# Kernel optimization log

Measured on AMD Instinct MI355X. Metric: run time of the kernel, lower is better.

The kernel has to match this reference:

```python
import jax, jax.numpy as jnp
import numpy as np

B, T, N, M = 128, 128, 32, 128  # batch, window(input_len), driving_series, hidden_size


def _lstm_cell(x_t, h, c, Wih, Whh, bih, bhh):
    # PyTorch gate order: i, f, g, o
    g = x_t @ Wih.T + bih + h @ Whh.T + bhh
    i, f, gg, o = jnp.split(g, 4, axis=-1)
    c = jax.nn.sigmoid(f) * c + jax.nn.sigmoid(i) * jnp.tanh(gg)
    h = jax.nn.sigmoid(o) * jnp.tanh(c)
    return h, c


def _lstm_seq(x, Wih, Whh, bih, bhh):
    # x: [B,T,n] -> outputs [B,T,m], zero init state
    Bc = x.shape[0]
    m = Whh.shape[1]
    def step(carry, x_t):
        h, c = carry
        h, c = _lstm_cell(x_t, h, c, Wih, Whh, bih, bhh)
        return (h, c), h
    h0 = jnp.zeros((Bc, m), x.dtype)
    (_, _), ys = jax.lax.scan(step, (h0, h0), jnp.swapaxes(x, 0, 1))
    return jnp.swapaxes(ys, 0, 1)


def _forward(x, Wih0, Whh0, bih0, bhh0, We, Ue, Ve,
             Wg, bg, Wa, ba,
             Wih1, Whh1, bih1, bhh1, Wih2, Whh2, bih2, bhh2):
    Bc, Tc, n = x.shape
    m = Whh0.shape[1]
    ux = jnp.einsum('btn,mn->btm', x, Ue)  # Ue(x), constant across steps

    def step(carry, x_t):
        h, c = carry
        hs = jnp.concatenate([h, c], axis=-1)              # [B,2m]
        e = jnp.tanh(ux + (hs @ We.T)[:, None, :]) @ Ve[0]  # [B,T]
        a = jax.nn.softmax(e, axis=1)
        ia_t = jnp.einsum('bt,btn->bn', a, x)              # attended input at step t
        h, c = _lstm_cell(x_t, h, c, Wih0, Whh0, bih0, bhh0)
        return (h, c), ia_t

    h0 = jnp.zeros((Bc, m), x.dtype)
    (_, _), ia = jax.lax.scan(step, (h0, h0), jnp.swapaxes(x, 0, 1))
    input_attention = jnp.swapaxes(ia, 0, 1)               # [B,T,n]

    # self (spatial) attention, fully vectorized over t
    g = jnp.tanh(jnp.einsum('btn,mn->btm', x, Wg) + bg)
    a = jax.nn.sigmoid(jnp.einsum('btm,nm->btn', g, Wa) + ba)
    self_attention = a * x                                  # [B,T,n]

    out1 = _lstm_seq(input_attention, Wih1, Whh1, bih1, bhh1)
    out2 = _lstm_seq(self_attention, Wih2, Whh2, bih2, bhh2)
    return jnp.concatenate([out1, out2], axis=-1)           # [B,T,2m]


def setup_inputs() -> dict:
    key = jax.random.key(0)
    ks = jax.random.split(key, 20)
    stdv = 1.0 / np.sqrt(M)
    u = lambda k, shp: jax.random.uniform(k, shp, jnp.float32, -stdv, stdv)
    inp = {
        'x': jax.random.normal(ks[0], (B, T, N), jnp.float32),
        'Wih0': u(ks[1], (4 * M, N)), 'Whh0': u(ks[2], (4 * M, M)),
        'bih0': u(ks[3], (4 * M,)), 'bhh0': u(ks[4], (4 * M,)),
        'We': u(ks[5], (M, 2 * M)), 'Ue': u(ks[6], (M, N)), 'Ve': u(ks[7], (1, M)),
        'Wg': u(ks[8], (M, N)), 'bg': u(ks[9], (M,)),
        'Wa': u(ks[10], (N, M)), 'ba': u(ks[11], (N,)),
        'Wih1': u(ks[12], (4 * M, N)), 'Whh1': u(ks[13], (4 * M, M)),
        'bih1': u(ks[14], (4 * M,)), 'bhh1': u(ks[15], (4 * M,)),
        'Wih2': u(ks[16], (4 * M, N)), 'Whh2': u(ks[17], (4 * M, M)),
        'bih2': u(ks[18], (4 * M,)), 'bhh2': u(ks[19], (4 * M,)),
    }
    return inp


def reference(x, Wih0, Whh0, bih0, bhh0, We, Ue, Ve, Wg, bg, Wa, ba,
              Wih1, Whh1, bih1, bhh1, Wih2, Whh2, bih2, bhh2):
    return _forward(x, Wih0, Whh0, bih0, bhh0, We, Ue, Ve, Wg, bg, Wa, ba,
                    Wih1, Whh1, bih1, bhh1, Wih2, Whh2, bih2, bhh2)
```

## Files before the change

kernel.cpp:

```cpp
#include <hip/hip_runtime.h>

#define DI __device__ __forceinline__

typedef _Float16 h2v __attribute__((ext_vector_type(2)));

DI float frcp(float v)  { return __builtin_amdgcn_rcpf(v); }
DI float fexp2(float v) { return __builtin_amdgcn_exp2f(v); }
DI float fsig(float v)  { return frcp(1.0f + __expf(-v)); }
DI float ftanh(float v) { return 1.0f - 2.0f * frcp(__expf(2.0f * v) + 1.0f); }
DI float dot4(float4 a, float4 b) { return a.x*b.x + a.y*b.y + a.z*b.z + a.w*b.w; }

DI h2v u2h(unsigned u) { return __builtin_bit_cast(h2v, u); }
DI unsigned pkrtz(float a, float b) {
    return __builtin_bit_cast(unsigned, __builtin_amdgcn_cvt_pkrtz(a, b));
}

DI float fdot2w(h2v a, h2v b, float c) {
#if __has_builtin(__builtin_amdgcn_fdot2)
    return __builtin_amdgcn_fdot2(a, b, c, false);
#else
    return c + (float)a.x * (float)b.x + (float)a.y * (float)b.y;
#endif
}

#define TWO_LOG2E 2.8853900817779268f

template <int MODE>
DI void lstm_scan4(const float* __restrict__ xin,
                   const float* __restrict__ Wih,
                   const float* __restrict__ Whh,
                   const float* __restrict__ bih,
                   const float* __restrict__ bhh,
                   float* __restrict__ rec,
                   float* __restrict__ outp,
                   float* lds)
{
    const int tid = threadIdx.x;
    const int r0 = tid & 127;
    const int kq = tid >> 7;
    unsigned* xp = (unsigned*)lds;
    unsigned* hp = (unsigned*)lds + 2048;
    float* pl = lds + 2112;

    for (int i = tid; i < 2048; i += 512) {
        const float2 v = *(const float2*)(xin + 2 * i);
        xp[i] = pkrtz(v.x, v.y);
    }
    if (tid < 64) hp[tid] = 0u;

    unsigned wpu[4][20];
    #pragma unroll
    for (int g = 0; g < 4; ++g) {
        const int r = g * 128 + r0;
        float4 wt[10];
        if (kq == 0) {
            const float4* pi4 = (const float4*)(Wih + r * 32);
            #pragma unroll
            for (int i = 0; i < 8; ++i) wt[i] = pi4[i];
            const float4* ph4 = (const float4*)(Whh + r * 128);
            wt[8] = ph4[0]; wt[9] = ph4[1];
        } else {
            const float4* ph4 = (const float4*)(Whh + r * 128 + 40 * kq - 32);
            #pragma unroll
            for (int i = 0; i < 10; ++i) wt[i] = ph4[i];
        }
        #pragma unroll
        for (int i = 0; i < 10; ++i) {
            wpu[g][2*i]   = pkrtz(wt[i].x, wt[i].y);
            wpu[g][2*i+1] = pkrtz(wt[i].z, wt[i].w);
        }
    }
    #pragma unroll
    for (int g = 0; g < 4; ++g)
        #pragma unroll
        for (int j = 0; j < 20; ++j)
            asm volatile("" : "+v"(wpu[g][j]));

    const int rr = tid >> 2;
    const int gg = tid & 3;
    const float bias = bih[gg * 128 + rr] + bhh[gg * 128 + rr];
    const float nl_a = (gg == 2) ? 2.0f : 1.0f;
    const float nl_b = (gg == 2) ? -1.0f : 0.0f;
    float hreg = 0.f, creg = 0.f;
    __syncthreads();

    for (int t = 0; t < 128; ++t) {
        uint4 z0, z1, z2, z3, ze;
        if (kq == 0) {
            const uint4* x4 = (const uint4*)(xp + t * 16);
            z0 = x4[0]; z1 = x4[1]; z2 = x4[2]; z3 = x4[3];
            ze = *(const uint4*)hp;
        } else {
            const uint4* h4 = (const uint4*)(hp + 20 * kq - 16);
            z0 = h4[0]; z1 = h4[1]; z2 = h4[2]; z3 = h4[3]; ze = h4[4];
        }
        float a0 = 0.f, a1 = 0.f, a2 = 0.f, a3 = 0.f;
        #define DG(J, U) { const h2v zz = u2h(U); \
            a0 = fdot2w(u2h(wpu[0][J]), zz, a0); \
            a1 = fdot2w(u2h(wpu[1][J]), zz, a1); \
            a2 = fdot2w(u2h(wpu[2][J]), zz, a2); \
            a3 = fdot2w(u2h(wpu[3][J]), zz, a3); }
        DG(0,  z0.x) DG(1,  z0.y) DG(2,  z0.z) DG(3,  z0.w)
        DG(4,  z1.x) DG(5,  z1.y) DG(6,  z1.z) DG(7,  z1.w)
        DG(8,  z2.x) DG(9,  z2.y) DG(10, z2.z) DG(11, z2.w)
        DG(12, z3.x) DG(13, z3.y) DG(14, z3.z) DG(15, z3.w)
        DG(16, ze.x) DG(17, ze.y) DG(18, ze.z) DG(19, ze.w)
        #undef DG
        pl[kq * 544 +       r0] = a0;
        pl[kq * 544 + 136 + r0] = a1;
        pl[kq * 544 + 272 + r0] = a2;
        pl[kq * 544 + 408 + r0] = a3;
        __syncthreads();

        float s = bias + pl[gg * 136 + rr]        + pl[544 + gg * 136 + rr]
                       + pl[1088 + gg * 136 + rr] + pl[1632 + gg * 136 + rr];
        float sg  = frcp(1.0f + __expf(-(nl_a * s)));
        float val = nl_a * sg + nl_b;
        float v1 = __shfl_xor(val, 1);
        float v2 = __shfl_xor(val, 2);
        float v3 = __shfl_xor(val, 3);
        float cn = v1 * creg + val * v2;
        float hn = v3 * ftanh(cn);
        float hn_hi = __shfl_down(hn, 4);
        if (gg == 0) {
            if (MODE == 0) {
                rec[t * 256 + rr]       = hreg;
                rec[t * 256 + 128 + rr] = creg;
            }
            creg = cn; hreg = hn;
            if (MODE == 1) outp[t * 256 + rr] = hn;
        }
        if ((tid & 7) == 0) hp[rr >> 1] = pkrtz(hn, hn_hi);
        __syncthreads();
    }
}

DI void selfatt_body(const float* __restrict__ x, const float* __restrict__ Wg,
                     const float* __restrict__ bg, const float* __restrict__ Wa,
                     const float* __restrict__ ba, float* __restrict__ sa,
                     int b, float* s)
{
    float* xl  = s;
    float* Wgl = s + 4224;
    float* WaT = s + 8448;
    float* bgl = s + 12672;
    float* bal = s + 12800;
    float* gl  = s + 12832;
    float* pp  = s + 13344;

    const int tid = threadIdx.x;
    for (int i = tid; i < 4096; i += 512) {
        int r = i >> 5, n = i & 31;
        xl[r * 33 + n]  = x[b * 4096 + i];
        Wgl[r * 33 + n] = Wg[i];
        WaT[(i & 127) * 33 + (i >> 7)] = Wa[i];
    }
    if (tid < 128) bgl[tid] = bg[tid];
    else if (tid < 160) bal[tid - 128] = ba[tid - 128];
    __syncthreads();

    const int tl = tid >> 7;
    for (int it = 0; it < 32; ++it) {
        {   const int m = tid & 127;
            const int t = it * 4 + tl;
            float acc = bgl[m];
            #pragma unroll
            for (int n = 0; n < 32; ++n) acc += xl[t * 33 + n] * Wgl[m * 33 + n];
            gl[tl * 128 + m] = ftanh(acc);
        }
        __syncthreads();
        {   const int n = tid & 31, c = (tid >> 5) & 3;
            float acc = 0.f;
            #pragma unroll
            for (int j = 0; j < 32; ++j) {
                int m = c * 32 + j;
                acc += gl[tl * 128 + m] * WaT[m * 33 + n];
            }
            pp[(tl * 4 + c) * 32 + n] = acc;
        }
        __syncthreads();
        if (tid < 128) {
            const int tl2 = tid >> 5, n = tid & 31;
            const int t = it * 4 + tl2;
            float sv = pp[(tl2 * 4 + 0) * 32 + n] + pp[(tl2 * 4 + 1) * 32 + n]
                     + pp[(tl2 * 4 + 2) * 32 + n] + pp[(tl2 * 4 + 3) * 32 + n] + bal[n];
            sa[b * 4096 + t * 32 + n] = fsig(sv) * xl[t * 33 + n];
        }
        __syncthreads();
    }
}

__global__ __launch_bounds__(512)
void k1_lstm0_sa(const float* __restrict__ x,
                 const float* __restrict__ Wih0, const float* __restrict__ Whh0,
                 const float* __restrict__ bih0, const float* __restrict__ bhh0,
                 const float* __restrict__ Wg, const float* __restrict__ bg,
                 const float* __restrict__ Wa, const float* __restrict__ ba,
                 float* __restrict__ rec, float* __restrict__ sa)
{
    __shared__ float smem[13856];
    const int blk = blockIdx.x;
    if (blk < 128) {
        lstm_scan4<0>(x + blk * 4096, Wih0, Whh0, bih0, bhh0,
                      rec + blk * 32768, nullptr, smem);
    } else {
        selfatt_body(x, Wg, bg, Wa, ba, sa, blk - 128, smem);
    }
}

__global__ __launch_bounds__(512)
void k3_lstm12(const float* __restrict__ ia, const float* __restrict__ sa,
               const float* __restrict__ Wih1, const float* __restrict__ Whh1,
               const float* __restrict__ bih1, const float* __restrict__ bhh1,
               const float* __restrict__ Wih2, const float* __restrict__ Whh2,
               const float* __restrict__ bih2, const float* __restrict__ bhh2,
               float* __restrict__ out)
{
    __shared__ float smem[4288];
    const int blk = blockIdx.x;
    if (blk < 128) {
        lstm_scan4<1>(ia + blk * 4096, Wih1, Whh1, bih1, bhh1,
                      nullptr, out + blk * 32768, smem);
    } else {
        const int b = blk - 128;
        lstm_scan4<1>(sa + b * 4096, Wih2, Whh2, bih2, bhh2,
                      nullptr, out + b * 32768 + 128, smem);
    }
}

__global__ __launch_bounds__(512, 1)
void kP_w2_sep(const float* __restrict__ We, const float* __restrict__ rec,
               float* __restrict__ w2)
{
    __shared__ float smem[12544];
    float* hsB  = smem;
    float* wbuf = smem + 8320;
    const int tid = threadIdx.x;
    const int b  = blockIdx.x >> 1;
    const int hh = blockIdx.x & 1;
    const int m = tid >> 2, q = tid & 3;

    float4 wer[16];
    {
        const float4* p = (const float4*)(We + m * 256 + q * 64);
        #pragma unroll
        for (int i = 0; i < 16; ++i) wer[i] = p[i];
    }
    #pragma unroll
    for (int i = 0; i < 16; i += 4) {
        asm volatile("" : "+v"(wer[i].x), "+v"(wer[i].y), "+v"(wer[i].z), "+v"(wer[i].w),
                          "+v"(wer[i+1].x), "+v"(wer[i+1].y), "+v"(wer[i+1].z), "+v"(wer[i+1].w),
                          "+v"(wer[i+2].x), "+v"(wer[i+2].y), "+v"(wer[i+2].z), "+v"(wer[i+2].w),
                          "+v"(wer[i+3].x), "+v"(wer[i+3].y), "+v"(wer[i+3].z), "+v"(wer[i+3].w));
    }

    for (int t2 = 0; t2 < 2; ++t2) {
        const int tb = hh * 2 + t2;
        __syncthreads();
        for (int i = tid; i < 8192; i += 512)
            hsB[(i >> 8) * 260 + (i & 255)] = rec[(long)b * 32768 + (tb * 32 + (i >> 8)) * 256 + (i & 255)];
        __syncthreads();
        for (int tl = 0; tl < 32; ++tl) {
            const float4* h4 = (const float4*)(hsB + tl * 260 + q * 64);
            float acc = 0.f;
            #pragma unroll
            for (int i = 0; i < 16; ++i) acc += dot4(wer[i], h4[i]);
            acc += __shfl_xor(acc, 1);
            acc += __shfl_xor(acc, 2);
            if (q == 0) wbuf[tl * 132 + m] = acc;
        }
        __syncthreads();
        for (int i = tid; i < 4096; i += 512)
            w2[(long)b * 16384 + tb * 4096 + i] = TWO_LOG2E * wbuf[(i >> 7) * 132 + (i & 127)];
    }
}

__global__ __launch_bounds__(512, 1)
void kP_w2_inplace(const float* __restrict__ We, float* __restrict__ rec)
{
    __shared__ float smem[12544];
    float* hsB  = smem;
    float* wbuf = smem + 8320;
    const int tid = threadIdx.x;
    const int b = blockIdx.x;
    const int m = tid >> 2, q = tid & 3;

    float4 wer[16];
    {
        const float4* p = (const float4*)(We + m * 256 + q * 64);
        #pragma unroll
        for (int i = 0; i < 16; ++i) wer[i] = p[i];
    }
    #pragma unroll
    for (int i = 0; i < 16; i += 4) {
        asm volatile("" : "+v"(wer[i].x), "+v"(wer[i].y), "+v"(wer[i].z), "+v"(wer[i].w),
                          "+v"(wer[i+1].x), "+v"(wer[i+1].y), "+v"(wer[i+1].z), "+v"(wer[i+1].w),
                          "+v"(wer[i+2].x), "+v"(wer[i+2].y), "+v"(wer[i+2].z), "+v"(wer[i+2].w),
                          "+v"(wer[i+3].x), "+v"(wer[i+3].y), "+v"(wer[i+3].z), "+v"(wer[i+3].w));
    }

    for (int tb = 0; tb < 4; ++tb) {
        __syncthreads();
        for (int i = tid; i < 8192; i += 512)
            hsB[(i >> 8) * 260 + (i & 255)] = rec[(long)b * 32768 + (tb * 32 + (i >> 8)) * 256 + (i & 255)];
        __syncthreads();
        for (int tl = 0; tl < 32; ++tl) {
            const float4* h4 = (const float4*)(hsB + tl * 260 + q * 64);
            float acc = 0.f;
            #pragma unroll
            for (int i = 0; i < 16; ++i) acc += dot4(wer[i], h4[i]);
            acc += __shfl_xor(acc, 1);
            acc += __shfl_xor(acc, 2);
            if (q == 0) wbuf[tl * 132 + m] = acc;
        }
        __syncthreads();
        for (int i = tid; i < 4096; i += 512)
            rec[(long)b * 32768 + tb * 4096 + i] = TWO_LOG2E * wbuf[(i >> 7) * 132 + (i & 127)];
    }
}

__global__ __launch_bounds__(512, 2)
void kB_attn(const float* __restrict__ x,
             const float* __restrict__ Ue,
             const float* __restrict__ Ve,
             const float* __restrict__ w2g,
             long bstr,
             float* __restrict__ ia)
{
    __shared__ float xl[4608];
    __shared__ float wl[4224];
    __shared__ float uxc[4224];
    __shared__ float UeAv[4608];
    __shared__ float vel[128];
    __shared__ float sinv[32];
    __shared__ float iap[576];

    const int tid = threadIdx.x;
    const int b  = blockIdx.x >> 2;
    const int tc = blockIdx.x & 3;

    for (int i = tid; i < 4096; i += 512) {
        xl[(i >> 5) * 36 + (i & 31)]   = x[b * 4096 + i];
        UeAv[(i >> 5) * 36 + (i & 31)] = Ue[i];
        wl[(i >> 7) * 132 + (i & 127)] = w2g[(long)b * bstr + (tc * 32 + (i >> 7)) * 128 + (i & 127)];
    }
    if (tid < 128) vel[tid] = 2.0f * Ve[tid];
    __syncthreads();

    const int ts = tid & 127, mg = tid >> 7;
    float4 xr[8];
    {
        const float4* xp = (const float4*)(xl + ts * 36);
        #pragma unroll
        for (int i = 0; i < 8; ++i) xr[i] = xp[i];
    }
    float VeTot = 0.f;
    for (int i = 0; i < 128; ++i) VeTot += vel[i];
    VeTot *= 0.5f;

    const int tp = tid >> 5, tg = tid & 31;
    const int t0 = 2 * tp, t1 = t0 + 1;
    float s0[4] = {0.f, 0.f, 0.f, 0.f};
    float s1[4] = {0.f, 0.f, 0.f, 0.f};

    for (int mc = 0; mc < 4; ++mc) {
        #pragma unroll
        for (int j = 0; j < 8; ++j) {
            const int ml = mg * 8 + j;
            const float4* u4 = (const float4*)(UeAv + (mc * 32 + ml) * 36);
            float acc = 0.f;
            #pragma unroll
            for (int i = 0; i < 8; ++i) acc += dot4(xr[i], u4[i]);
            uxc[ml * 132 + ts] = TWO_LOG2E * acc;
        }
        __syncthreads();
        #pragma unroll 8
        for (int ml = 0; ml < 32; ++ml) {
            const int m = mc * 32 + ml;
            const float vm = vel[m];
            const float w0 = wl[t0 * 132 + m];
            const float w1 = wl[t1 * 132 + m];
            const float4 u4 = *(const float4*)(uxc + ml * 132 + 4 * tg);
            s0[0] += vm * frcp(fexp2(u4.x + w0) + 1.0f);
            s0[1] += vm * frcp(fexp2(u4.y + w0) + 1.0f);
            s0[2] += vm * frcp(fexp2(u4.z + w0) + 1.0f);
            s0[3] += vm * frcp(fexp2(u4.w + w0) + 1.0f);
            s1[0] += vm * frcp(fexp2(u4.x + w1) + 1.0f);
            s1[1] += vm * frcp(fexp2(u4.y + w1) + 1.0f);
            s1[2] += vm * frcp(fexp2(u4.z + w1) + 1.0f);
            s1[3] += vm * frcp(fexp2(u4.w + w1) + 1.0f);
        }
        __syncthreads();
    }

    float e0[4], e1[4];
    #pragma unroll
    for (int j = 0; j < 4; ++j) { e0[j] = VeTot - s0[j]; e1[j] = VeTot - s1[j]; }
    float M0 = fmaxf(fmaxf(e0[0], e0[1]), fmaxf(e0[2], e0[3]));
    float M1 = fmaxf(fmaxf(e1[0], e1[1]), fmaxf(e1[2], e1[3]));
    #pragma unroll
    for (int o = 1; o < 32; o <<= 1) {
        M0 = fmaxf(M0, __shfl_xor(M0, o));
        M1 = fmaxf(M1, __shfl_xor(M1, o));
    }
    float a00 = __expf(e0[0] - M0), a01 = __expf(e0[1] - M0);
    float a02 = __expf(e0[2] - M0), a03 = __expf(e0[3] - M0);
    float a10 = __expf(e1[0] - M1), a11 = __expf(e1[1] - M1);
    float a12 = __expf(e1[2] - M1), a13 = __expf(e1[3] - M1);
    float S0 = a00 + a01 + a02 + a03;
    float S1 = a10 + a11 + a12 + a13;
    #pragma unroll
    for (int o = 1; o < 32; o <<= 1) {
        S0 += __shfl_xor(S0, o);
        S1 += __shfl_xor(S1, o);
    }
    float* av = UeAv;
    *(float4*)(av + t0 * 128 + 4 * tg) = make_float4(a00, a01, a02, a03);
    *(float4*)(av + t1 * 128 + 4 * tg) = make_float4(a10, a11, a12, a13);
    if (tg == 0) { sinv[t0] = frcp(S0); sinv[t1] = frcp(S1); }
    __syncthreads();

    const int gph = tid >> 5, n = tid & 31;
    for (int tl = 0; tl < 32; ++tl) {
        float acc = 0.f;
        #pragma unroll
        for (int j = 0; j < 8; ++j)
            acc += av[tl * 128 + gph * 8 + j] * xl[(gph * 8 + j) * 36 + n];
        iap[gph * 36 + n] = acc;
        __syncthreads();
        if (tid < 32) {
            float s = 0.f;
            #pragma unroll
            for (int g = 0; g < 16; ++g) s += iap[g * 36 + tid];
            ia[((long)(b * 128 + tc * 32 + tl)) * 32 + tid] = s * sinv[tl];
        }
        __syncthreads();
    }
}

extern "C" void kernel_launch(void* const* d_in, const int* in_sizes, int n_in,
                              void* d_out, int out_size, void* d_ws, size_t ws_size,
                              hipStream_t stream)
{
    const float* x    = (const float*)d_in[0];
    const float* Wih0 = (const float*)d_in[1];
    const float* Whh0 = (const float*)d_in[2];
    const float* bih0 = (const float*)d_in[3];
    const float* bhh0 = (const float*)d_in[4];
    const float* We   = (const float*)d_in[5];
    const float* Ue   = (const float*)d_in[6];
    const float* Ve   = (const float*)d_in[7];
    const float* Wg   = (const float*)d_in[8];
    const float* bg   = (const float*)d_in[9];
    const float* Wa   = (const float*)d_in[10];
    const float* ba   = (const float*)d_in[11];
    const float* Wih1 = (const float*)d_in[12];
    const float* Whh1 = (const float*)d_in[13];
    const float* bih1 = (const float*)d_in[14];
    const float* bhh1 = (const float*)d_in[15];
    const float* Wih2 = (const float*)d_in[16];
    const float* Whh2 = (const float*)d_in[17];
    const float* bih2 = (const float*)d_in[18];
    const float* bhh2 = (const float*)d_in[19];

    float* out = (float*)d_out;
    float* ws  = (float*)d_ws;
    float* sa  = ws;
    float* rec = ws + 524288;
    float* iaw = ws + 4718592;
    float* w2  = ws + 5242880;
    const bool sep = ws_size >= (size_t)7340032 * 4;

    k1_lstm0_sa<<<256, 512, 0, stream>>>(x, Wih0, Whh0, bih0, bhh0,
                                         Wg, bg, Wa, ba, rec, sa);
    if (sep) {
        kP_w2_sep<<<256, 512, 0, stream>>>(We, rec, w2);
        kB_attn<<<512, 512, 0, stream>>>(x, Ue, Ve, w2, 16384L, iaw);
    } else {
        kP_w2_inplace<<<128, 512, 0, stream>>>(We, rec);
        kB_attn<<<512, 512, 0, stream>>>(x, Ue, Ve, rec, 32768L, iaw);
    }
    k3_lstm12<<<256, 512, 0, stream>>>(iaw, sa, Wih1, Whh1, bih1, bhh1,
                                       Wih2, Whh2, bih2, bhh2, out);
}
```

Before: 447.9 us.

## Batch 16 sequences per block and run LSTM recurrences on MFMA

The LSTM scans now go through MFMA 16x16x32 f16 instructions, with each block handling 16 batch rows instead of one sequence per block. Whh stays in registers as packed halves, Wih lives in LDS, and the next x step is prefetched during the current one. The self-attention blocks are split into two halves along time so the first kernel keeps enough blocks. The aim is to replace per-thread fdot2 accumulation and an LDS partial-sum reduction with matrix-core throughput. The trade-off is far fewer blocks (8 or 16 for the LSTMs), so the serial recurrence latency per step decides the runtime and much of the GPU sits idle.

After: 454.1 us. No clear change (+1.4%).

```diff
diff --git a/kernel.cpp b/kernel.cpp
--- a/kernel.cpp
+++ b/kernel.cpp
@@ -2,7 +2,9 @@
 
 #define DI __device__ __forceinline__
 
-typedef _Float16 h2v __attribute__((ext_vector_type(2)));
+typedef _Float16 h2v  __attribute__((ext_vector_type(2)));
+typedef _Float16 half8 __attribute__((ext_vector_type(8)));
+typedef float    f32x4 __attribute__((ext_vector_type(4)));
 
 DI float frcp(float v)  { return __builtin_amdgcn_rcpf(v); }
 DI float fexp2(float v) { return __builtin_amdgcn_exp2f(v); }
@@ -14,145 +16,150 @@
 DI unsigned pkrtz(float a, float b) {
     return __builtin_bit_cast(unsigned, __builtin_amdgcn_cvt_pkrtz(a, b));
 }
-
-DI float fdot2w(h2v a, h2v b, float c) {
-#if __has_builtin(__builtin_amdgcn_fdot2)
-    return __builtin_amdgcn_fdot2(a, b, c, false);
-#else
-    return c + (float)a.x * (float)b.x + (float)a.y * (float)b.y;
-#endif
-}
+DI half8 u2h8(uint4 v) { return __builtin_bit_cast(half8, v); }
 
 #define TWO_LOG2E 2.8853900817779268f
 
 template <int MODE>
-DI void lstm_scan4(const float* __restrict__ xin,
-                   const float* __restrict__ Wih,
-                   const float* __restrict__ Whh,
-                   const float* __restrict__ bih,
-                   const float* __restrict__ bhh,
-                   float* __restrict__ rec,
-                   float* __restrict__ outp,
-                   float* lds)
+DI void lstm_mfma(const float* __restrict__ xin,
+                  const float* __restrict__ Wih,
+                  const float* __restrict__ Whh,
+                  const float* __restrict__ bih,
+                  const float* __restrict__ bhh,
+                  float* __restrict__ rec,
+                  float* __restrict__ outp,
+                  unsigned* lds)
 {
     const int tid = threadIdx.x;
-    const int r0 = tid & 127;
-    const int kq = tid >> 7;
-    unsigned* xp = (unsigned*)lds;
-    unsigned* hp = (unsigned*)lds + 2048;
-    float* pl = lds + 2112;
-
-    for (int i = tid; i < 2048; i += 512) {
-        const float2 v = *(const float2*)(xin + 2 * i);
-        xp[i] = pkrtz(v.x, v.y);
-    }
-    if (tid < 64) hp[tid] = 0u;
-
-    unsigned wpu[4][20];
-    #pragma unroll
-    for (int g = 0; g < 4; ++g) {
-        const int r = g * 128 + r0;
-        float4 wt[10];
-        if (kq == 0) {
-            const float4* pi4 = (const float4*)(Wih + r * 32);
-            #pragma unroll
-            for (int i = 0; i < 8; ++i) wt[i] = pi4[i];
-            const float4* ph4 = (const float4*)(Whh + r * 128);
-            wt[8] = ph4[0]; wt[9] = ph4[1];
-        } else {
-            const float4* ph4 = (const float4*)(Whh + r * 128 + 40 * kq - 32);
-            #pragma unroll
-            for (int i = 0; i < 10; ++i) wt[i] = ph4[i];
-        }
-        #pragma unroll
-        for (int i = 0; i < 10; ++i) {
-            wpu[g][2*i]   = pkrtz(wt[i].x, wt[i].y);
-            wpu[g][2*i+1] = pkrtz(wt[i].z, wt[i].w);
-        }
-    }
-    #pragma unroll
-    for (int g = 0; g < 4; ++g)
-        #pragma unroll
-        for (int j = 0; j < 20; ++j)
-            asm volatile("" : "+v"(wpu[g][j]));
-
-    const int rr = tid >> 2;
-    const int gg = tid & 3;
-    const float bias = bih[gg * 128 + rr] + bhh[gg * 128 + rr];
-    const float nl_a = (gg == 2) ? 2.0f : 1.0f;
-    const float nl_b = (gg == 2) ? -1.0f : 0.0f;
-    float hreg = 0.f, creg = 0.f;
+    const int l  = tid & 63;
+    const int w  = tid >> 6;
+    const int lr = l & 15;
+    const int lg = l >> 4;
+
+    unsigned* Z  = lds;
+    unsigned* WX = lds + 1344;
+
+    uint4 whA[4][4];
+    #pragma unroll
+    for (int j = 0; j < 4; ++j) {
+        const int g = 128*j + 16*w + lr;
+        #pragma unroll
+        for (int kt = 1; kt <= 4; ++kt) {
+            const float4* p = (const float4*)(Whh + g*128 + (kt-1)*32 + lg*8);
+            const float4 a = p[0], b2 = p[1];
+            whA[j][kt-1] = make_uint4(pkrtz(a.x,a.y), pkrtz(a.z,a.w),
+                                      pkrtz(b2.x,b2.y), pkrtz(b2.z,b2.w));
+        }
+        const float4* q = (const float4*)(Wih + g*32 + lg*8);
+        const float4 a = q[0], b2 = q[1];
+        *(uint4*)(WX + ((w*4 + j)*64 + l)*4) =
+            make_uint4(pkrtz(a.x,a.y), pkrtz(a.z,a.w), pkrtz(b2.x,b2.y), pkrtz(b2.z,b2.w));
+    }
+    #pragma unroll
+    for (int j = 0; j < 4; ++j)
+        #pragma unroll
+        for (int kt = 0; kt < 4; ++kt)
+            asm volatile("" : "+v"(whA[j][kt].x), "+v"(whA[j][kt].y),
+                               "+v"(whA[j][kt].z), "+v"(whA[j][kt].w));
+
+    unsigned bp[8];
+    #pragma unroll
+    for (int j = 0; j < 4; ++j) {
+        const int g0 = 128*j + 16*w + lg*4;
+        bp[2*j]   = pkrtz(bih[g0]   + bhh[g0],   bih[g0+1] + bhh[g0+1]);
+        bp[2*j+1] = pkrtz(bih[g0+2] + bhh[g0+2], bih[g0+3] + bhh[g0+3]);
+    }
+    #pragma unroll
+    for (int j = 0; j < 8; ++j) asm volatile("" : "+v"(bp[j]));
+
+    float cst[4] = {0.f,0.f,0.f,0.f}, hst[4] = {0.f,0.f,0.f,0.f};
+
+    if (tid < 256) {
+        const int b = tid >> 4, i = tid & 15;
+        const float2 v = *(const float2*)(xin + b*4096 + 2*i);
+        Z[b*84 + i] = pkrtz(v.x, v.y);
+    }
+    for (int i = tid; i < 1024; i += 512)
+        Z[(i >> 6)*84 + 16 + (i & 63)] = 0u;
     __syncthreads();
 
+    const int zrd = lr*84 + lg*4;
+    const int zwr = lr*84 + 16 + 8*w + lg*2;
+
     for (int t = 0; t < 128; ++t) {
-        uint4 z0, z1, z2, z3, ze;
-        if (kq == 0) {
-            const uint4* x4 = (const uint4*)(xp + t * 16);
-            z0 = x4[0]; z1 = x4[1]; z2 = x4[2]; z3 = x4[3];
-            ze = *(const uint4*)hp;
-        } else {
-            const uint4* h4 = (const uint4*)(hp + 20 * kq - 16);
-            z0 = h4[0]; z1 = h4[1]; z2 = h4[2]; z3 = h4[3]; ze = h4[4];
-        }
-        float a0 = 0.f, a1 = 0.f, a2 = 0.f, a3 = 0.f;
-        #define DG(J, U) { const h2v zz = u2h(U); \
-            a0 = fdot2w(u2h(wpu[0][J]), zz, a0); \
-            a1 = fdot2w(u2h(wpu[1][J]), zz, a1); \
-            a2 = fdot2w(u2h(wpu[2][J]), zz, a2); \
-            a3 = fdot2w(u2h(wpu[3][J]), zz, a3); }
-        DG(0,  z0.x) DG(1,  z0.y) DG(2,  z0.z) DG(3,  z0.w)
-        DG(4,  z1.x) DG(5,  z1.y) DG(6,  z1.z) DG(7,  z1.w)
-        DG(8,  z2.x) DG(9,  z2.y) DG(10, z2.z) DG(11, z2.w)
-        DG(12, z3.x) DG(13, z3.y) DG(14, z3.z) DG(15, z3.w)
-        DG(16, ze.x) DG(17, ze.y) DG(18, ze.z) DG(19, ze.w)
-        #undef DG
-        pl[kq * 544 +       r0] = a0;
-        pl[kq * 544 + 136 + r0] = a1;
-        pl[kq * 544 + 272 + r0] = a2;
-        pl[kq * 544 + 408 + r0] = a3;
-        __syncthreads();
-
-        float s = bias + pl[gg * 136 + rr]        + pl[544 + gg * 136 + rr]
-                       + pl[1088 + gg * 136 + rr] + pl[1632 + gg * 136 + rr];
-        float sg  = frcp(1.0f + __expf(-(nl_a * s)));
-        float val = nl_a * sg + nl_b;
-        float v1 = __shfl_xor(val, 1);
-        float v2 = __shfl_xor(val, 2);
-        float v3 = __shfl_xor(val, 3);
-        float cn = v1 * creg + val * v2;
-        float hn = v3 * ftanh(cn);
-        float hn_hi = __shfl_down(hn, 4);
-        if (gg == 0) {
-            if (MODE == 0) {
-                rec[t * 256 + rr]       = hreg;
-                rec[t * 256 + 128 + rr] = creg;
+        float2 xf = make_float2(0.f, 0.f);
+        if (tid < 256 && t < 127)
+            xf = *(const float2*)(xin + (tid>>4)*4096 + (t+1)*32 + 2*(tid&15));
+
+        f32x4 acc[4];
+        #pragma unroll
+        for (int j = 0; j < 4; ++j) {
+            const h2v p0 = u2h(bp[2*j]), p1 = u2h(bp[2*j+1]);
+            acc[j] = (f32x4){(float)p0.x, (float)p0.y, (float)p1.x, (float)p1.y};
+        }
+        {
+            const uint4 bf = *(const uint4*)(Z + zrd);
+            const half8 B = u2h8(bf);
+            #pragma unroll
+            for (int j = 0; j < 4; ++j) {
+                const uint4 af = *(const uint4*)(WX + ((w*4 + j)*64 + l)*4);
+                acc[j] = __builtin_amdgcn_mfma_f32_16x16x32_f16(u2h8(af), B, acc[j], 0, 0, 0);
             }
-            creg = cn; hreg = hn;
-            if (MODE == 1) outp[t * 256 + rr] = hn;
-        }
-        if ((tid & 7) == 0) hp[rr >> 1] = pkrtz(hn, hn_hi);
-        __syncthreads();
-    }
-}
-
-DI void selfatt_body(const float* __restrict__ x, const float* __restrict__ Wg,
+        }
+        #pragma unroll
+        for (int kt = 1; kt <= 4; ++kt) {
+            const uint4 bf = *(const uint4*)(Z + zrd + kt*16);
+            const half8 B = u2h8(bf);
+            #pragma unroll
+            for (int j = 0; j < 4; ++j)
+                acc[j] = __builtin_amdgcn_mfma_f32_16x16x32_f16(u2h8(whA[j][kt-1]), B, acc[j], 0, 0, 0);
+        }
+
+        const int u0 = 16*w + lg*4;
+        if (MODE == 0) {
+            *(float4*)(rec + lr*32768 + t*256 + u0)       = make_float4(hst[0],hst[1],hst[2],hst[3]);
+            *(float4*)(rec + lr*32768 + t*256 + 128 + u0) = make_float4(cst[0],cst[1],cst[2],cst[3]);
+        }
+        #pragma unroll
+        for (int e = 0; e < 4; ++e) {
+            const float iv = fsig(acc[0][e]);
+            const float fv = fsig(acc[1][e]);
+            const float gv = ftanh(acc[2][e]);
+            const float ov = fsig(acc[3][e]);
+            cst[e] = fv*cst[e] + iv*gv;
+            hst[e] = ov*ftanh(cst[e]);
+        }
+        if (MODE == 1)
+            *(float4*)(outp + lr*32768 + t*256 + u0) = make_float4(hst[0],hst[1],hst[2],hst[3]);
+
+        __syncthreads();
+        *(uint2*)(Z + zwr) = make_uint2(pkrtz(hst[0],hst[1]), pkrtz(hst[2],hst[3]));
+        if (tid < 256 && t < 127)
+            Z[(tid>>4)*84 + (tid&15)] = pkrtz(xf.x, xf.y);
+        __syncthreads();
+    }
+}
+
+DI void selfatt_half(const float* __restrict__ x, const float* __restrict__ Wg,
                      const float* __restrict__ bg, const float* __restrict__ Wa,
                      const float* __restrict__ ba, float* __restrict__ sa,
-                     int b, float* s)
+                     int b, int hf, float* s)
 {
     float* xl  = s;
-    float* Wgl = s + 4224;
-    float* WaT = s + 8448;
-    float* bgl = s + 12672;
-    float* bal = s + 12800;
-    float* gl  = s + 12832;
-    float* pp  = s + 13344;
+    float* Wgl = s + 2112;
+    float* WaT = s + 6336;
+    float* bgl = s + 10560;
+    float* bal = s + 10688;
+    float* gl  = s + 10720;
+    float* pp  = s + 11232;
 
     const int tid = threadIdx.x;
+    for (int i = tid; i < 2048; i += 512) {
+        const int r = i >> 5, n = i & 31;
+        xl[r * 33 + n] = x[b * 4096 + (hf * 64 + r) * 32 + n];
+    }
     for (int i = tid; i < 4096; i += 512) {
-        int r = i >> 5, n = i & 31;
-        xl[r * 33 + n]  = x[b * 4096 + i];
-        Wgl[r * 33 + n] = Wg[i];
+        Wgl[(i >> 5) * 33 + (i & 31)] = Wg[i];
         WaT[(i & 127) * 33 + (i >> 7)] = Wa[i];
     }
     if (tid < 128) bgl[tid] = bg[tid];
@@ -160,12 +167,12 @@
     __syncthreads();
 
     const int tl = tid >> 7;
-    for (int it = 0; it < 32; ++it) {
+    for (int it = 0; it < 16; ++it) {
         {   const int m = tid & 127;
-            const int t = it * 4 + tl;
+            const int tloc = it * 4 + tl;
             float acc = bgl[m];
             #pragma unroll
-            for (int n = 0; n < 32; ++n) acc += xl[t * 33 + n] * Wgl[m * 33 + n];
+            for (int n = 0; n < 32; ++n) acc += xl[tloc * 33 + n] * Wgl[m * 33 + n];
             gl[tl * 128 + m] = ftanh(acc);
         }
         __syncthreads();
@@ -173,7 +180,7 @@
             float acc = 0.f;
             #pragma unroll
             for (int j = 0; j < 32; ++j) {
-                int m = c * 32 + j;
+                const int m = c * 32 + j;
                 acc += gl[tl * 128 + m] * WaT[m * 33 + n];
             }
             pp[(tl * 4 + c) * 32 + n] = acc;
@@ -181,10 +188,10 @@
         __syncthreads();
         if (tid < 128) {
             const int tl2 = tid >> 5, n = tid & 31;
-            const int t = it * 4 + tl2;
-            float sv = pp[(tl2 * 4 + 0) * 32 + n] + pp[(tl2 * 4 + 1) * 32 + n]
-                     + pp[(tl2 * 4 + 2) * 32 + n] + pp[(tl2 * 4 + 3) * 32 + n] + bal[n];
-            sa[b * 4096 + t * 32 + n] = fsig(sv) * xl[t * 33 + n];
+            const int tloc = it * 4 + tl2;
+            const float sv = pp[(tl2*4+0)*32+n] + pp[(tl2*4+1)*32+n]
+                           + pp[(tl2*4+2)*32+n] + pp[(tl2*4+3)*32+n] + bal[n];
+            sa[b * 4096 + (hf * 64 + tloc) * 32 + n] = fsig(sv) * xl[tloc * 33 + n];
         }
         __syncthreads();
     }
@@ -198,13 +205,15 @@
                  const float* __restrict__ Wa, const float* __restrict__ ba,
                  float* __restrict__ rec, float* __restrict__ sa)
 {
-    __shared__ float smem[13856];
+    __shared__ float smem[11744];
     const int blk = blockIdx.x;
-    if (blk < 128) {
-        lstm_scan4<0>(x + blk * 4096, Wih0, Whh0, bih0, bhh0,
-                      rec + blk * 32768, nullptr, smem);
+    if (blk < 8) {
+        const long bbase = (long)blk * 16;
+        lstm_mfma<0>(x + bbase * 4096, Wih0, Whh0, bih0, bhh0,
+                     rec + bbase * 32768, nullptr, (unsigned*)smem);
     } else {
-        selfatt_body(x, Wg, bg, Wa, ba, sa, blk - 128, smem);
+        const int idx = blk - 8;
+        selfatt_half(x, Wg, bg, Wa, ba, sa, idx >> 1, idx & 1, smem);
     }
 }
 
@@ -216,15 +225,16 @@
                const float* __restrict__ bih2, const float* __restrict__ bhh2,
                float* __restrict__ out)
 {
-    __shared__ float smem[4288];
+    __shared__ float smem[9536];
     const int blk = blockIdx.x;
-    if (blk < 128) {
-        lstm_scan4<1>(ia + blk * 4096, Wih1, Whh1, bih1, bhh1,
-                      nullptr, out + blk * 32768, smem);
+    if (blk < 8) {
+        const long bbase = (long)blk * 16;
+        lstm_mfma<1>(ia + bbase * 4096, Wih1, Whh1, bih1, bhh1,
+                     nullptr, out + bbase * 32768, (unsigned*)smem);
     } else {
-        const int b = blk - 128;
-        lstm_scan4<1>(sa + b * 4096, Wih2, Whh2, bih2, bhh2,
-                      nullptr, out + b * 32768 + 128, smem);
+        const long bbase = (long)(blk - 8) * 16;
+        lstm_mfma<1>(sa + bbase * 4096, Wih2, Whh2, bih2, bhh2,
+                     nullptr, out + bbase * 32768 + 128, (unsigned*)smem);
     }
 }
 
@@ -471,7 +481,7 @@
     float* w2  = ws + 5242880;
     const bool sep = ws_size >= (size_t)7340032 * 4;
 
-    k1_lstm0_sa<<<256, 512, 0, stream>>>(x, Wih0, Whh0, bih0, bhh0,
+    k1_lstm0_sa<<<264, 512, 0, stream>>>(x, Wih0, Whh0, bih0, bhh0,
                                          Wg, bg, Wa, ba, rec, sa);
     if (sep) {
         kP_w2_sep<<<256, 512, 0, stream>>>(We, rec, w2);
@@ -480,6 +490,6 @@
         kP_w2_inplace<<<128, 512, 0, stream>>>(We, rec);
         kB_attn<<<512, 512, 0, stream>>>(x, Ue, Ve, rec, 32768L, iaw);
     }
-    k3_lstm12<<<256, 512, 0, stream>>>(iaw, sa, Wih1, Whh1, bih1, bhh1,
-                                       Wih2, Whh2, bih2, bhh2, out);
-}
+    k3_lstm12<<<16, 512, 0, stream>>>(iaw, sa, Wih1, Whh1, bih1, bhh1,
+                                      Wih2, Whh2, bih2, bhh2, out);
+}
```
